# Performance work log

Hardware: AMD Instinct MI355X
Metric: run time of the kernel (lower is better)

## Reference

```python
import jax, jax.numpy as jnp
import numpy as np

EPS = 1e-5
SLOPE = 0.2

def _lrelu(x):
    return jnp.where(x >= 0, x, SLOPE * x)

def _bn(x, axes):
    # BatchNorm in training mode with gamma=1, beta=0 (module defaults), biased var
    m = jnp.mean(x, axis=axes, keepdims=True)
    v = jnp.var(x, axis=axes, keepdims=True)
    return (x - m) * jax.lax.rsqrt(v + EPS)

def _knn(x, k):
    # x: [B, C, N] -> idx [B, N, k] of nearest neighbors (incl. self)
    inner = -2.0 * jnp.einsum('bcn,bcm->bnm', x, x)
    xx = jnp.sum(x * x, axis=1)  # [B, N]
    d = -xx[:, :, None] - inner - xx[:, None, :]  # negative squared dist
    return jax.lax.top_k(d, k)[1]

def _graph_feature(x, k):
    # x: [B, C, N] -> [B, 2C, N, k] of (neighbor - center, center)
    idx = _knn(x, k)                       # [B, N, k]
    xt = jnp.transpose(x, (0, 2, 1))       # [B, N, C]
    feat = jax.vmap(lambda xb, ib: xb[ib])(xt, idx)  # [B, N, k, C]
    center = xt[:, :, None, :]
    out = jnp.concatenate([feat - center, jnp.broadcast_to(center, feat.shape)], axis=-1)
    return jnp.transpose(out, (0, 3, 1, 2))

def _conv2(w, x):   # 1x1 conv2d: x [B,C,N,K]
    return jnp.einsum('oc,bcnk->bonk', w, x)

def _conv1(w, x):   # 1x1 conv1d: x [B,C,N]
    return jnp.einsum('oc,bcn->bon', w, x)

def _pool(xyz, feature, wp, bp, kp):
    # dropout is identity in eval mode
    proj = _conv1(wp, feature) + bp[None, :, None]     # [B, C, N]
    vector = jnp.max(proj, axis=-1, keepdims=True)     # [B, C, 1]
    scores = jax.nn.sigmoid(jnp.sum(feature * vector, axis=1))  # [B, N]
    values, idx = jax.lax.top_k(scores, kp)            # [B, kp]
    node_static = jnp.take_along_axis(xyz, idx[:, None, :], axis=2)
    node_feature = jnp.take_along_axis(feature, idx[:, None, :], axis=2)
    v = values[:, None, :]
    return node_static * v, node_feature * v


def setup_inputs() -> dict:
    key = jax.random.key(0)
    ks = jax.random.split(key, 20)
    def rn(i, shape, s=0.05):
        return jax.random.normal(ks[i], shape, dtype=jnp.float32) * s
    return {
        'x': jax.random.normal(ks[0], (16, 3, 2048), dtype=jnp.float32),
        'w1': rn(1, (64, 6)), 'w2': rn(2, (64, 128)), 'w2m': rn(3, (1024, 128)),
        'w3': rn(4, (128, 256)), 'w4': rn(5, (128, 256)), 'w4m': rn(6, (1024, 256)),
        'w5': rn(7, (256, 512)), 'w5m': rn(8, (1024, 256)),
        'wp1': rn(9, (128, 128)), 'bp1': rn(10, (128,)),
        'wp2': rn(11, (256, 256)), 'bp2': rn(12, (256,)),
        'wl1': rn(13, (512, 3072)),
        'wl2': rn(14, (256, 512)), 'bl2': rn(15, (256,)),
        'wl3': rn(16, (40, 256)), 'bl3': rn(17, (40,)),
    }


def reference(x, w1, w2, w2m, w3, w4, w4m, w5, w5m, wp1, bp1, wp2, bp2, wl1, wl2, bl2, wl3, bl3):
    k = 20
    xyz = x
    # stage 1 (N=2048)
    h = _lrelu(_bn(_conv2(w1, _graph_feature(x, k)), (0, 2, 3)))
    x1 = jnp.max(h, axis=-1)                       # [B, 64, N]
    h = _lrelu(_bn(_conv2(w2, _graph_feature(x1, k)), (0, 2, 3)))
    x2 = jnp.max(h, axis=-1)                       # [B, 64, N]
    xt1_ = jnp.concatenate([x1, x2], axis=1)       # [B, 128, N]
    xt1 = _lrelu(_bn(_conv1(w2m, xt1_), (0, 2)))   # [B, 1024, N]
    node1, nf1 = _pool(xyz, xt1_, wp1, bp1, 256)   # [B,3,256], [B,128,256]
    # stage 2 (256 nodes, k//2)
    h = _lrelu(_bn(_conv2(w3, _graph_feature(nf1, k // 2)), (0, 2, 3)))
    x3 = jnp.max(h, axis=-1)                       # [B, 128, 256]
    h = _lrelu(_bn(_conv2(w4, _graph_feature(x3, k // 2)), (0, 2, 3)))
    x4 = jnp.max(h, axis=-1)
    xt2_ = jnp.concatenate([x3, x4], axis=1)       # [B, 256, 256]
    xt2 = _lrelu(_bn(_conv1(w4m, xt2_), (0, 2)))   # [B, 1024, 256]
    node2, nf2 = _pool(node1, xt2_, wp2, bp2, 64)  # [B,3,64], [B,256,64]
    # stage 3 (64 nodes, k//4)
    h = _lrelu(_bn(_conv2(w5, _graph_feature(nf2, k // 4)), (0, 2, 3)))
    x5 = jnp.max(h, axis=-1)                       # [B, 256, 64]
    xt3 = _lrelu(_bn(_conv1(w5m, x5), (0, 2)))     # [B, 1024, 64]
    # global max pools + head (dropout = identity in eval)
    g = jnp.concatenate([jnp.max(xt1, -1), jnp.max(xt2, -1), jnp.max(xt3, -1)], axis=1)  # [B, 3072]
    h = _lrelu(_bn(g @ wl1.T, (0,)))
    h = _lrelu(_bn(h @ wl2.T + bl2, (0,)))
    out = h @ wl3.T + bl3                          # [B, 40]
    return (out, node1, node2)
```

## Files before the change

kernel.cpp:

```cpp
#include <hip/hip_runtime.h>
#include <cmath>
#include <cstdint>
#include <cstddef>

typedef unsigned int u32;
typedef unsigned short u16;
typedef unsigned long long u64;
typedef __attribute__((ext_vector_type(8))) short short8v;
typedef __attribute__((ext_vector_type(4))) float f32x4;

#define TPB 256
#define EPSV 1e-5f
#define SLP 0.2f

__device__ __forceinline__ float lrelu(float x){ return x >= 0.f ? x : SLP*x; }
__device__ __forceinline__ u32 encf(float f){ u32 u=__float_as_uint(f); return (u&0x80000000u)? ~u : (u|0x80000000u); }
__device__ __forceinline__ float decf(u32 e){ return (e&0x80000000u)? __uint_as_float(e&0x7FFFFFFFu) : __uint_as_float(~e); }
__device__ __forceinline__ u16 f2b(float f){ u32 u=__float_as_uint(f); return (u16)((u + 0x7FFFu + ((u>>16)&1u))>>16); }
__device__ __forceinline__ float b2f(u16 h){ return __uint_as_float(((u32)h)<<16); }

__global__ void k_detect(const u16* __restrict__ raw, int n, int* __restrict__ flag){
  __shared__ float red[TPB];
  int tid=threadIdx.x; float m=0.f;
  for(int i=tid;i<n;i+=TPB){
    float v=fabsf(b2f(raw[i]));
    if(!isnan(v) && !isinf(v) && v>m) m=v;
  }
  red[tid]=m; __syncthreads();
  for(int s=TPB/2;s>0;s>>=1){ if(tid<s) red[tid]=fmaxf(red[tid],red[tid+s]); __syncthreads(); }
  if(tid==0) *flag = (red[0] > 1000.f) ? 1 : 0;
}

struct CvtArgs{ const void* s[18]; float* d[18]; int n[18]; };
__global__ void k_cvt_all(CvtArgs a, const int* __restrict__ flag){
  int z=blockIdx.y; int n=a.n[z]; int f=*flag;
  const void* s=a.s[z]; float* d=a.d[z];
  for(int i=blockIdx.x*TPB+threadIdx.x; i<n; i+=gridDim.x*TPB)
    d[i] = f ? ((const float*)s)[i] : b2f(((const u16*)s)[i]);
}

__global__ void k_castw(const float* __restrict__ W, u16* __restrict__ Wb, int n){
  int i=blockIdx.x*TPB+threadIdx.x; if(i<n) Wb[i]=f2b(W[i]);
}

__global__ void k_xpose_bf(const float* __restrict__ X, u16* __restrict__ Xb,
                           int ldC, int C, int N){
  __shared__ float t[32][33];
  int b=blockIdx.z;
  int c0=blockIdx.y*32, n0=blockIdx.x*32;
  int tx=threadIdx.x&31, ty=threadIdx.x>>5;
  const float* Xs = X + (size_t)b*ldC*N;
  #pragma unroll
  for(int i=0;i<4;i++){
    int c=c0+ty+i*8;
    t[ty+i*8][tx] = (c<C && n0+tx<N) ? Xs[(size_t)c*N + n0+tx] : 0.f;
  }
  __syncthreads();
  u16* Ob = Xb + (size_t)b*N*C;
  #pragma unroll
  for(int i=0;i<4;i++){
    int n=n0+ty+i*8;
    if(n<N && c0+tx<C) Ob[(size_t)n*C + c0+tx] = f2b(t[tx][ty+i*8]);
  }
}

template<int KSTEPS>
__global__ __launch_bounds__(256) void k_convmax_mfma(
    const u16* __restrict__ Wb, const u16* __restrict__ Xb,
    u32* __restrict__ gmaxEnc, int gstride, int g_off, double* __restrict__ stats,
    int C, int N, int O){
  int tid=threadIdx.x, lane=tid&63, w=tid>>6;
  int b=blockIdx.z;
  int oW = blockIdx.y*64 + w*16;
  int nB = blockIdx.x*256;
  int row16 = lane&15, grp = lane>>4;
  short8v af[KSTEPS];
  const u16* Wrow = Wb + (size_t)(oW + row16)*C + grp*8;
  #pragma unroll
  for(int ks=0;ks<KSTEPS;ks++) af[ks] = *(const short8v*)(Wrow + ks*32);
  const short8v zb = {0,0,0,0,0,0,0,0};
  f32x4 acc[16];
  #pragma unroll
  for(int t=0;t<16;t++){
    int n = nB + t*16 + row16;
    bool nv = (n < N);
    const u16* Xrow = Xb + ((size_t)b*N + (nv? n:0))*C + grp*8;
    short8v bf[KSTEPS];
    #pragma unroll
    for(int ks=0;ks<KSTEPS;ks++) bf[ks] = nv ? *(const short8v*)(Xrow + ks*32) : zb;
    f32x4 a = {0.f,0.f,0.f,0.f};
    #pragma unroll
    for(int ks=0;ks<KSTEPS;ks++)
      a = __builtin_amdgcn_mfma_f32_16x16x32_bf16(af[ks], bf[ks], a, 0, 0, 0);
    acc[t]=a;
  }
  float mxr[4], s1r[4], s2r[4];
  #pragma unroll
  for(int r=0;r<4;r++){ mxr[r]=-INFINITY; s1r[r]=0.f; s2r[r]=0.f; }
  #pragma unroll
  for(int t=0;t<16;t++){
    int n = nB + t*16 + row16;
    bool nv = (n<N);
    #pragma unroll
    for(int r=0;r<4;r++){
      float y = acc[t][r];
      if(nv){ mxr[r]=fmaxf(mxr[r],y); s1r[r]+=y; s2r[r]+=y*y; }
    }
  }
  #pragma unroll
  for(int s=1;s<16;s<<=1){
    #pragma unroll
    for(int r=0;r<4;r++){
      mxr[r]=fmaxf(mxr[r], __shfl_xor(mxr[r], s));
      s1r[r]+=__shfl_xor(s1r[r], s);
      s2r[r]+=__shfl_xor(s2r[r], s);
    }
  }
  if(row16==0){
    #pragma unroll
    for(int r=0;r<4;r++){
      int o = oW + grp*4 + r;
      atomicMax(&gmaxEnc[(size_t)b*gstride + g_off + o], encf(mxr[r]));
      atomicAdd(&stats[2*o], (double)s1r[r]);
      atomicAdd(&stats[2*o+1], (double)s2r[r]);
    }
  }
}

__global__ void k_sqnorm(const float* __restrict__ X, float* __restrict__ xx, int B, int ldC, int C, int N){
  int i=blockIdx.x*TPB+threadIdx.x; if(i>=B*N) return;
  int b=i/N, n=i-b*N;
  const float* p = X + ((size_t)b*ldC)*N + n;
  float s=0.f;
  for(int c=0;c<C;c++){ float x=p[(size_t)c*N]; s+=x*x; }
  xx[i]=s;
}

template<int JMAX, int CT>
__global__ __launch_bounds__(256) void k_knn_fused(
    const float* __restrict__ X, const float* __restrict__ xx,
    int ldC, int KSEL, int* __restrict__ idxOut){
  const int N = JMAX*64;
  extern __shared__ float sm[];
  __shared__ u64 cand[4][128];
  int tid=threadIdx.x, lane=tid&63, w=tid>>6;
  int b=blockIdx.y, row0=blockIdx.x*4;
  const float* Xb = X + (size_t)b*ldC*N;
  const float* xxb = xx + (size_t)b*N;

  if constexpr (JMAX==32){
    int c0 = tid*4;
    float4 acc0[4], acc1[4];
    #pragma unroll
    for(int r=0;r<4;r++){ acc0[r]=make_float4(0,0,0,0); acc1[r]=make_float4(0,0,0,0); }
    #pragma unroll 4
    for(int c=0;c<CT;c++){
      const float* Xc = Xb + (size_t)c*N;
      float4 b0 = *(const float4*)&Xc[c0];
      float4 b1 = *(const float4*)&Xc[c0+1024];
      #pragma unroll
      for(int r=0;r<4;r++){
        float a = Xc[row0+r];
        acc0[r].x += a*b0.x; acc0[r].y += a*b0.y; acc0[r].z += a*b0.z; acc0[r].w += a*b0.w;
        acc1[r].x += a*b1.x; acc1[r].y += a*b1.y; acc1[r].z += a*b1.z; acc1[r].w += a*b1.w;
      }
    }
    float4 xm0 = *(const float4*)&xxb[c0];
    float4 xm1 = *(const float4*)&xxb[c0+1024];
    #pragma unroll
    for(int r=0;r<4;r++){
      float xr = xxb[row0+r];
      float4 d0, d1;
      d0.x=2.f*acc0[r].x-xr-xm0.x; d0.y=2.f*acc0[r].y-xr-xm0.y;
      d0.z=2.f*acc0[r].z-xr-xm0.z; d0.w=2.f*acc0[r].w-xr-xm0.w;
      d1.x=2.f*acc1[r].x-xr-xm1.x; d1.y=2.f*acc1[r].y-xr-xm1.y;
      d1.z=2.f*acc1[r].z-xr-xm1.z; d1.w=2.f*acc1[r].w-xr-xm1.w;
      *(float4*)&sm[r*N + c0]        = d0;
      *(float4*)&sm[r*N + c0 + 1024] = d1;
    }
  } else {
    int tcol = (tid < N)? tid : (tid & (N-1));
    float acc[4];
    #pragma unroll
    for(int r=0;r<4;r++) acc[r]=0.f;
    #pragma unroll 4
    for(int c=0;c<CT;c++){
      const float* Xc = Xb + (size_t)c*N;
      float bv = Xc[tcol];
      #pragma unroll
      for(int r=0;r<4;r++) acc[r] += Xc[row0+r]*bv;
    }
    float xm = xxb[tcol];
    #pragma unroll
    for(int r=0;r<4;r++) sm[r*N + tcol] = 2.f*acc[r] - xxb[row0+r] - xm;
  }
  __syncthreads();

  u64* cw = cand[w];
  int r = w;
  const float* Sr = sm + (size_t)r*N;
  u32 ev[JMAX];
  if constexpr (JMAX>=4){
    #pragma unroll
    for(int ch=0;ch<JMAX/4;ch++){
      float4 v = *(const float4*)&Sr[ch*256 + lane*4];
      ev[ch*4+0]=encf(v.x); ev[ch*4+1]=encf(v.y); ev[ch*4+2]=encf(v.z); ev[ch*4+3]=encf(v.w);
    }
  } else {
    ev[0]=encf(Sr[lane]);
  }
  int* op = idxOut + ((size_t)b*N + row0 + r)*KSEL;
  if constexpr (JMAX>=8){
    u32 vmax=ev[0];
    #pragma unroll
    for(int j=1;j<JMAX;j++) vmax = vmax>ev[j]? vmax:ev[j];
    u32 lo=0u, hi=0xFFFFFFFFu;
    while(lo<hi){
      u32 d=hi-lo; u32 mid=lo+(d>>1)+(d&1u);
      int cnum=(int)__popcll(__ballot(vmax>=mid));
      if(cnum>=KSEL) lo=mid; else hi=mid-1u;
    }
    u32 T=lo;
    u64 lml=((u64)1<<lane)-1ull;
    u32 base=0;
    #pragma unroll
    for(int j=0;j<JMAX;j++){
      bool p = ev[j]>=T;
      u64 mk=__ballot(p);
      u32 pos=base+(u32)__popcll(mk&lml);
      int m = (j>>2)*256 + lane*4 + (j&3);
      if(p && pos<128u) cw[pos] = ((u64)ev[j]<<32) | (u64)(u32)(~(u32)m);
      base += (u32)__popcll(mk);
    }
    int nc=(int)base;
    if(nc<=64){
      u64 cv = cw[lane];
      if(lane>=nc) cv=0ull;
      #pragma unroll
      for(int kk=2;kk<=64;kk<<=1){
        #pragma unroll
        for(int jj=kk>>1;jj>0;jj>>=1){
          u64 p=__shfl_xor(cv,jj);
          bool takeMax=(((lane&jj)!=0)==((lane&kk)==0));
          u64 mx=cv>p?cv:p, mn=cv>p?p:cv;
          cv=takeMax?mx:mn;
        }
      }
      if(lane>=64-KSEL) op[63-lane]=(int)(~(u32)cv);
    } else if(nc<=128){
      u64 c0v=cw[lane], c1v=cw[64+lane];
      if(64+lane>=nc) c1v=0ull;
      u64 kl=~0ull;
      for(int t=0;t<KSEL;t++){
        u64 bk=(c0v<kl)?c0v:0ull;
        if(c1v<kl&&c1v>bk) bk=c1v;
        #pragma unroll
        for(int s=1;s<64;s<<=1){u64 ok=__shfl_xor(bk,s); if(ok>bk)bk=ok;}
        if(lane==0) op[t]=(int)(~(u32)bk);
        kl=bk;
      }
    } else {
      u64 kl=~0ull;
      for(int t=0;t<KSEL;t++){
        u64 bk=0ull;
        #pragma unroll
        for(int j=0;j<JMAX;j++){
          int m = (j>>2)*256 + lane*4 + (j&3);
          u64 kj=((u64)ev[j]<<32)|(u64)(u32)(~(u32)m);
          if(kj<kl&&kj>bk) bk=kj;
        }
        #pragma unroll
        for(int s=1;s<64;s<<=1){u64 ok=__shfl_xor(bk,s); if(ok>bk)bk=ok;}
        if(lane==0) op[t]=(int)(~(u32)bk);
        kl=bk;
      }
    }
  } else {
    u64 key[JMAX];
    #pragma unroll
    for(int j=0;j<JMAX;j++){
      int m = (JMAX>=4)? ((j>>2)*256 + lane*4 + (j&3)) : lane;
      key[j]=((u64)ev[j]<<32)|(u64)(u32)(~(u32)m);
    }
    u64 kl=~0ull;
    for(int t=0;t<KSEL;t++){
      u64 bk=0ull;
      #pragma unroll
      for(int j=0;j<JMAX;j++){ u64 kj=key[j]; if(kj<kl&&kj>bk) bk=kj; }
      #pragma unroll
      for(int s=1;s<64;s<<=1){u64 ok=__shfl_xor(bk,s); if(ok>bk)bk=ok;}
      if(lane==0) op[t]=(int)(~(u32)bk);
      kl=bk;
    }
  }
}

__global__ void k_topk_sort(const float* __restrict__ S, int M, int K,
                            int* __restrict__ idxOut, float* __restrict__ valOut){
  extern __shared__ u64 key[];
  int b=blockIdx.x, tid=threadIdx.x;
  const float* Sr = S + (size_t)b*M;
  for(int i=tid;i<M;i+=TPB)
    key[i] = ((u64)(~encf(Sr[i]))<<32) | (u32)i;
  __syncthreads();
  for(int k=2;k<=M;k<<=1){
    for(int j=k>>1;j>0;j>>=1){
      for(int i=tid;i<M;i+=TPB){
        int ixj=i^j;
        if(ixj>i){
          u64 a=key[i], c=key[ixj];
          bool up=((i&k)==0);
          if(up ? (a>c) : (a<c)){ key[i]=c; key[ixj]=a; }
        }
      }
      __syncthreads();
    }
  }
  for(int p=tid;p<K;p+=TPB){
    u64 kk=key[p];
    idxOut[(size_t)b*K+p]=(int)(u32)(kk&0xFFFFFFFFull);
    valOut[(size_t)b*K+p]=decf(~(u32)(kk>>32));
  }
}

__global__ void k_uv(const float* __restrict__ X, int ldC, const float* __restrict__ W,
                     float* __restrict__ U, float* __restrict__ V, int C, int N, int O){
  int n=blockIdx.x*TPB+threadIdx.x; if(n>=N) return;
  int o=blockIdx.y, b=blockIdx.z;
  const float* Xb = X + ((size_t)b*ldC)*N + n;
  const float* Wr = W + (size_t)o*2*C;
  float u=0,v=0;
  for(int c=0;c<C;c++){ float x=Xb[(size_t)c*N]; float wa=Wr[c], wb=Wr[C+c]; u+=wa*x; v+=(wb-wa)*x; }
  size_t off=((size_t)b*O+o)*N+n; U[off]=u; V[off]=v;
}

template<int KT, int OT>
__global__ void k_nbr_t(const float* __restrict__ U, const float* __restrict__ V, const int* __restrict__ idx,
                        float* __restrict__ outBase, int ldCout, int ch_off,
                        double* __restrict__ stats, int O, int N){
  __shared__ double redS[4][OT], redQ[4][OT];
  int tid=threadIdx.x, lane=tid&63, wv=tid>>6;
  int n = blockIdx.x*TPB+tid;
  int o0 = blockIdx.y*OT, b = blockIdx.z;
  bool act = (n<N);
  int nc = act? n : (N-1);
  int jr[KT];
  const int* jp = idx + ((size_t)b*N+nc)*KT;
  #pragma unroll
  for(int k=0;k<KT;k++){ int j=jp[k]; jr[k] = ((unsigned)j<(unsigned)N)? j : 0; }
  for(int oo=0;oo<OT;oo++){
    const float* Ur = U + ((size_t)b*O+o0+oo)*N;
    float mx=-INFINITY, s1=0.f, s2=0.f;
    #pragma unroll
    for(int k=0;k<KT;k++){ float u=Ur[jr[k]]; mx=fmaxf(mx,u); s1+=u; s2+=u*u; }
    float v = V[((size_t)b*O+o0+oo)*N+nc];
    if(act) outBase[((size_t)b*ldCout+ch_off+o0+oo)*N+n] = mx+v;
    double cs = act ? ((double)s1 + (double)KT*(double)v) : 0.0;
    double cq = act ? ((double)s2 + 2.0*(double)v*(double)s1 + (double)KT*(double)v*(double)v) : 0.0;
    #pragma unroll
    for(int s=1;s<64;s<<=1){ cs += __shfl_xor(cs,s); cq += __shfl_xor(cq,s); }
    if(lane==0){ redS[wv][oo]=cs; redQ[wv][oo]=cq; }
  }
  __syncthreads();
  if(tid<OT){
    double s=0,q=0;
    #pragma unroll
    for(int w=0;w<4;w++){ s+=redS[w][tid]; q+=redQ[w][tid]; }
    atomicAdd(&stats[2*(o0+tid)], s);
    atomicAdd(&stats[2*(o0+tid)+1], q);
  }
}

__global__ void k_bnact(float* __restrict__ out, int ldCout, int ch_off, const double* __restrict__ stats,
                        int O, int N, double cnt){
  int n=blockIdx.x*TPB+threadIdx.x; if(n>=N) return;
  int o=blockIdx.y, b=blockIdx.z;
  double m=stats[2*o]/cnt;
  double var=stats[2*o+1]/cnt - m*m;
  float s=rsqrtf((float)var+EPSV);
  size_t p=((size_t)b*ldCout+ch_off+o)*N+n;
  float h=out[p];
  out[p] = lrelu((float)((double)h-m)*s);
}

template<int PTS>
__global__ void k_convmax(const float* __restrict__ X, int ldC, const float* __restrict__ W, const float* __restrict__ bias,
                          u32* __restrict__ gmaxEnc, int gstride, int g_off, double* __restrict__ stats,
                          int C, int N, int O){
  __shared__ float red[4*16*3];
  int tid=threadIdx.x, ot=blockIdx.y, b=blockIdx.z;
  int lane=tid&63, wv=tid>>6;
  int n0 = blockIdx.x*TPB*PTS + tid*PTS;
  bool act = (n0 < N);
  int n0c = act ? n0 : (N-PTS);
  const float* Xb = X + ((size_t)b*ldC)*N;
  const float* Wr = W + (size_t)ot*16*C;
  float acc[16][PTS];
  #pragma unroll
  for(int oo=0;oo<16;oo++)
    #pragma unroll
    for(int p=0;p<PTS;p++) acc[oo][p]=0.f;
  for(int c=0;c<C;c+=4){
    float xv[4][PTS];
    #pragma unroll
    for(int cc=0;cc<4;cc++){
      if(PTS==4){
        float4 t = *(const float4*)&Xb[(size_t)(c+cc)*N + n0c];
        xv[cc][0]=t.x; xv[cc][1]=t.y; xv[cc][2]=t.z; xv[cc][3]=t.w;
      } else {
        xv[cc][0]=Xb[(size_t)(c+cc)*N + n0c];
      }
    }
    #pragma unroll
    for(int oo=0;oo<16;oo++){
      float w0=Wr[oo*C+c], w1=Wr[oo*C+c+1], w2=Wr[oo*C+c+2], w3=Wr[oo*C+c+3];
      #pragma unroll
      for(int p=0;p<PTS;p++)
        acc[oo][p] += w0*xv[0][p] + w1*xv[1][p] + w2*xv[2][p] + w3*xv[3][p];
    }
  }
  bool hs = (stats!=nullptr);
  #pragma unroll
  for(int oo=0;oo<16;oo++){
    float bval = bias? bias[ot*16+oo] : 0.f;
    float mx=-INFINITY, s1=0.f, s2=0.f;
    #pragma unroll
    for(int p=0;p<PTS;p++){
      float y=acc[oo][p]+bval;
      if(act && n0+p<N){ mx=fmaxf(mx,y); s1+=y; s2+=y*y; }
    }
    #pragma unroll
    for(int s=1;s<64;s<<=1){
      mx=fmaxf(mx,__shfl_xor(mx,s));
      if(hs){ s1+=__shfl_xor(s1,s); s2+=__shfl_xor(s2,s); }
    }
    if(lane==0){ red[(wv*16+oo)*3]=mx; red[(wv*16+oo)*3+1]=s1; red[(wv*16+oo)*3+2]=s2; }
  }
  __syncthreads();
  if(tid<16){
    int oo=tid, o=ot*16+oo;
    float mx=red[oo*3], s1=red[oo*3+1], s2=red[oo*3+2];
    #pragma unroll
    for(int w=1;w<4;w++){ mx=fmaxf(mx,red[(w*16+oo)*3]); s1+=red[(w*16+oo)*3+1]; s2+=red[(w*16+oo)*3+2]; }
    atomicMax(&gmaxEnc[(size_t)b*gstride+g_off+o], encf(mx));
    if(hs){ atomicAdd(&stats[2*o],(double)s1); atomicAdd(&stats[2*o+1],(double)s2); }
  }
}

__global__ void k_gfinal(const u32* __restrict__ gmaxEnc, int gstride, int g_off, const double* __restrict__ stats,
                         float* __restrict__ G, int B, int O, double cnt){
  int i=blockIdx.x*TPB+threadIdx.x; if(i>=B*O) return;
  int b=i/O, o=i-b*O;
  double m=stats[2*o]/cnt;
  double var=stats[2*o+1]/cnt - m*m;
  float s=rsqrtf((float)var+EPSV);
  float x=decf(gmaxEnc[(size_t)b*gstride+g_off+o]);
  G[(size_t)b*gstride+g_off+o]=lrelu((float)((double)x-m)*s);
}

__global__ void k_scores(const float* __restrict__ X, int ldC, const u32* __restrict__ vecEnc,
                         float* __restrict__ sc, int C, int N){
  int n=blockIdx.x*TPB+threadIdx.x; if(n>=N) return;
  int b=blockIdx.y;
  const float* Xb = X + ((size_t)b*ldC)*N + n;
  double s=0;
  for(int c=0;c<C;c++) s += (double)Xb[(size_t)c*N]*(double)decf(vecEnc[(size_t)b*C+c]);
  float sf=(float)s;
  sc[(size_t)b*N+n]=1.f/(1.f+expf(-sf));
}

__global__ void k_pgather(const float* __restrict__ xyz, int ldCx, const float* __restrict__ feat, int ldCf,
                          const int* __restrict__ pidx, const float* __restrict__ pval,
                          float* __restrict__ nodeOut, float* __restrict__ nfOut, int Cf, int Nin, int Kp){
  int b=blockIdx.y;
  int i=blockIdx.x*TPB+threadIdx.x;
  int total=(3+Cf)*Kp; if(i>=total) return;
  int c=i/Kp, p=i-c*Kp;
  int j=pidx[(size_t)b*Kp+p]; if((unsigned)j>=(unsigned)Nin) j=0;
  float v=pval[(size_t)b*Kp+p];
  if(c<3) nodeOut[((size_t)b*3+c)*Kp+p]=xyz[((size_t)b*ldCx+c)*Nin+j]*v;
  else { int cf=c-3; nfOut[((size_t)b*Cf+cf)*Kp+p]=feat[((size_t)b*ldCf+cf)*Nin+j]*v; }
}

__global__ void k_fc_wave(const float* __restrict__ A, const float* __restrict__ W, const float* __restrict__ bias,
                          float* __restrict__ Y, int B, int IN, int OUT){
  int gw = (blockIdx.x*blockDim.x + threadIdx.x) >> 6;
  if(gw >= B*OUT) return;
  int lane = threadIdx.x & 63;
  int b = gw/OUT, j = gw - b*OUT;
  const float4* a4 = (const float4*)(A + (size_t)b*IN);
  const float4* w4 = (const float4*)(W + (size_t)j*IN);
  int n4 = IN >> 2;
  float s = 0.f;
  for(int t=lane; t<n4; t+=64){
    float4 av=a4[t], wv=w4[t];
    s += av.x*wv.x + av.y*wv.y + av.z*wv.z + av.w*wv.w;
  }
  #pragma unroll
  for(int sh=1; sh<64; sh<<=1) s += __shfl_xor(s, sh);
  if(lane==0) Y[gw] = s + (bias? bias[j]:0.f);
}

__global__ void k_bnb(const float* __restrict__ Y, float* __restrict__ H, int B, int F){
  int f=blockIdx.x*TPB+threadIdx.x; if(f>=F) return;
  double s=0,q=0;
  for(int b=0;b<B;b++){ double y=Y[(size_t)b*F+f]; s+=y; q+=y*y; }
  double m=s/B, var=q/B-m*m;
  float sc=rsqrtf((float)var+EPSV);
  for(int b=0;b<B;b++){ float y=Y[(size_t)b*F+f]; H[(size_t)b*F+f]=lrelu((float)((double)y-m)*sc); }
}

__global__ void k_out(const float* __restrict__ OUTF, const float* __restrict__ N1v, const float* __restrict__ N2v,
                      void* __restrict__ dout, const int* __restrict__ flag){
  int i=blockIdx.x*TPB+threadIdx.x; if(i>=16000) return;
  float v = (i<640)? OUTF[i] : (i<12928)? N1v[i-640] : N2v[i-12928];
  if(*flag) ((float*)dout)[i]=v; else ((u16*)dout)[i]=f2b(v);
}

extern "C" void kernel_launch(void* const* d_in, const int* in_sizes, int n_in,
                              void* d_out, int out_size, void* d_ws, size_t ws_size,
                              hipStream_t stream){
  const int B=16;
  char* basep=(char*)d_ws; size_t off=0;
  auto alloc=[&](size_t elems, size_t esz)->void*{
    off=(off+255)&~(size_t)255; void* p=basep+off; off+=elems*esz; return p;
  };
  const int NINP=18;
  const int insz[NINP]={98304,384,8192,131072,32768,32768,262144,131072,262144,16384,128,65536,256,1572864,131072,256,10240,40};
  float* F[NINP];
  for(int i=0;i<NINP;i++) F[i]=(float*)alloc((size_t)insz[i],4);
  float* XF=F[0];
  float *W1F=F[1],*W2F=F[2],*W2MF=F[3],*W3F=F[4],*W4F=F[5],*W4MF=F[6],*W5F=F[7],*W5MF=F[8],
        *WP1F=F[9],*BP1F=F[10],*WP2F=F[11],*BP2F=F[12],*WL1F=F[13],*WL2F=F[14],*BL2F=F[15],*WL3F=F[16],*BL3F=F[17];
  float* XX  =(float*)alloc((size_t)16*2048,4);
  float* U   =(float*)alloc((size_t)16*64*2048,4);
  float* V   =(float*)alloc((size_t)16*64*2048,4);
  float* XT1 =(float*)alloc((size_t)16*128*2048,4);
  float* XT2 =(float*)alloc((size_t)16*256*256,4);
  float* NF1 =(float*)alloc((size_t)16*128*256,4);
  float* NF2 =(float*)alloc((size_t)16*256*64,4);
  float* X5  =(float*)alloc((size_t)16*256*64,4);
  float* NODE1=(float*)alloc((size_t)16*3*256,4);
  float* NODE2=(float*)alloc((size_t)16*3*64,4);
  float* SCORES=(float*)alloc((size_t)16*2048,4);
  float* PVAL1=(float*)alloc((size_t)16*256,4);
  float* PVAL2=(float*)alloc((size_t)16*64,4);
  float* G   =(float*)alloc((size_t)16*3072,4);
  float* Y1  =(float*)alloc((size_t)16*512,4);
  float* H1  =(float*)alloc((size_t)16*512,4);
  float* Y2  =(float*)alloc((size_t)16*256,4);
  float* H2  =(float*)alloc((size_t)16*256,4);
  float* OUTF=(float*)alloc((size_t)16*40,4);
  u32* GMAX  =(u32*)alloc((size_t)16*3072,4);
  u32* VECENC=(u32*)alloc((size_t)16*256,4);
  int* IDX   =(int*)alloc((size_t)16*2048*20,4);
  int* PIDX1 =(int*)alloc((size_t)16*256,4);
  int* PIDX2 =(int*)alloc((size_t)16*64,4);
  double* STATS=(double*)alloc((size_t)2*1024,8);
  int* FLAG  =(int*)alloc(64,4);
  u16* XTB  =(u16*)alloc((size_t)16*2048*128,2);
  u16* WB2M =(u16*)alloc((size_t)131072,2);
  u16* WB4M =(u16*)alloc((size_t)262144,2);
  u16* WB5M =(u16*)alloc((size_t)262144,2);

  k_detect<<<dim3(1),dim3(TPB),0,stream>>>((const u16*)d_in[1], insz[1], FLAG);
  CvtArgs ca;
  for(int i=0;i<NINP;i++){ ca.s[i]=d_in[i]; ca.d[i]=F[i]; ca.n[i]=insz[i]; }
  k_cvt_all<<<dim3(64,NINP),dim3(TPB),0,stream>>>(ca, FLAG);
  k_castw<<<dim3((131072+TPB-1)/TPB),dim3(TPB),0,stream>>>(W2MF,WB2M,131072);
  k_castw<<<dim3((262144+TPB-1)/TPB),dim3(TPB),0,stream>>>(W4MF,WB4M,262144);
  k_castw<<<dim3((262144+TPB-1)/TPB),dim3(TPB),0,stream>>>(W5MF,WB5M,262144);

  auto knn=[&](const float* X, int ldC, int C, int N, int K){
    k_sqnorm<<<dim3((B*N+TPB-1)/TPB),dim3(TPB),0,stream>>>(X,XX,B,ldC,C,N);
    size_t shm=(size_t)4*N*4;
    if(N==2048 && C==3)       k_knn_fused<32,3>  <<<dim3(N/4,B),dim3(256),shm,stream>>>(X,XX,ldC,K,IDX);
    else if(N==2048)          k_knn_fused<32,64> <<<dim3(N/4,B),dim3(256),shm,stream>>>(X,XX,ldC,K,IDX);
    else if(N==256)           k_knn_fused<4,128> <<<dim3(N/4,B),dim3(256),shm,stream>>>(X,XX,ldC,K,IDX);
    else                      k_knn_fused<1,256> <<<dim3(N/4,B),dim3(256),shm,stream>>>(X,XX,ldC,K,IDX);
  };

  auto graph_conv=[&](const float* X, int ldC, int C, int N, int K, const float* W, int O,
                      float* outBase, int ldCout, int ch_off){
    knn(X,ldC,C,N,K);
    k_uv<<<dim3((N+TPB-1)/TPB,O,B),dim3(TPB),0,stream>>>(X,ldC,W,U,V,C,N,O);
    hipMemsetAsync(STATS,0,2*(size_t)O*sizeof(double),stream);
    dim3 g((N+TPB-1)/TPB, O/8, B);
    if(K==20)      k_nbr_t<20,8><<<g,dim3(TPB),0,stream>>>(U,V,IDX,outBase,ldCout,ch_off,STATS,O,N);
    else if(K==10) k_nbr_t<10,8><<<g,dim3(TPB),0,stream>>>(U,V,IDX,outBase,ldCout,ch_off,STATS,O,N);
    else           k_nbr_t<5,8> <<<g,dim3(TPB),0,stream>>>(U,V,IDX,outBase,ldCout,ch_off,STATS,O,N);
    double cnt=(double)B*(double)N*(double)K;
    k_bnact<<<dim3((N+TPB-1)/TPB,O,B),dim3(TPB),0,stream>>>(outBase,ldCout,ch_off,STATS,O,N,cnt);
  };

  auto convmax_f32=[&](const float* X,int ldC,const float* W,const float* bias,
                   u32* gmax,int gstride,int g_off,double* stats,int C,int N,int O){
    if(N>=1024) k_convmax<4><<<dim3((N+TPB*4-1)/(TPB*4),O/16,B),dim3(TPB),0,stream>>>(X,ldC,W,bias,gmax,gstride,g_off,stats,C,N,O);
    else        k_convmax<1><<<dim3((N+TPB-1)/TPB,O/16,B),dim3(TPB),0,stream>>>(X,ldC,W,bias,gmax,gstride,g_off,stats,C,N,O);
  };

  auto pool=[&](const float* xyzF,int ldCx,const float* featF,int ldCf,int Cf,int Nin,
                const float* WP,const float* BP,int Op,int Kp,
                float* nodeOut,float* nfOut,int* pidx,float* pval){
    hipMemsetAsync(VECENC,0,(size_t)B*Op*4,stream);
    convmax_f32(featF,ldCf,WP,BP,VECENC,Op,0,(double*)nullptr,Cf,Nin,Op);
    k_scores<<<dim3((Nin+TPB-1)/TPB,B),dim3(TPB),0,stream>>>(featF,ldCf,VECENC,SCORES,Cf,Nin);
    k_topk_sort<<<dim3(B),dim3(TPB),(size_t)Nin*8,stream>>>(SCORES,Nin,Kp,pidx,pval);
    k_pgather<<<dim3(((3+Cf)*Kp+TPB-1)/TPB,B),dim3(TPB),0,stream>>>(xyzF,ldCx,featF,ldCf,pidx,pval,nodeOut,nfOut,Cf,Nin,Kp);
  };

  auto gseg=[&](const float* X,int ldC,int C,int N,const u16* WBc,int g_off,double cnt){
    hipMemsetAsync(STATS,0,2*1024*sizeof(double),stream);
    k_xpose_bf<<<dim3((N+31)/32,(C+31)/32,B),dim3(256),0,stream>>>(X,XTB,ldC,C,N);
    dim3 g((N+255)/256, 1024/64, B);
    if(C==128) k_convmax_mfma<4><<<g,dim3(256),0,stream>>>(WBc,XTB,GMAX,3072,g_off,STATS,C,N,1024);
    else       k_convmax_mfma<8><<<g,dim3(256),0,stream>>>(WBc,XTB,GMAX,3072,g_off,STATS,C,N,1024);
    k_gfinal<<<dim3((B*1024+TPB-1)/TPB),dim3(TPB),0,stream>>>(GMAX,3072,g_off,STATS,G,B,1024,cnt);
  };

  graph_conv(XF,3,3,2048,20,W1F,64,XT1,128,0);
  graph_conv(XT1,128,64,2048,20,W2F,64,XT1,128,64);
  hipMemsetAsync(GMAX,0,(size_t)16*3072*4,stream);
  gseg(XT1,128,128,2048,WB2M,0,(double)16*2048);
  pool(XF,3,XT1,128,128,2048,WP1F,BP1F,128,256,NODE1,NF1,PIDX1,PVAL1);
  graph_conv(NF1,128,128,256,10,W3F,128,XT2,256,0);
  graph_conv(XT2,256,128,256,10,W4F,128,XT2,256,128);
  gseg(XT2,256,256,256,WB4M,1024,(double)16*256);
  pool(NODE1,3,XT2,256,256,256,WP2F,BP2F,256,64,NODE2,NF2,PIDX2,PVAL2);
  graph_conv(NF2,256,256,64,5,W5F,256,X5,256,0);
  gseg(X5,256,256,64,WB5M,2048,(double)16*64);
  k_fc_wave<<<dim3((16*512*64+TPB-1)/TPB),dim3(TPB),0,stream>>>(G,WL1F,(const float*)nullptr,Y1,16,3072,512);
  k_bnb<<<dim3((512+TPB-1)/TPB),dim3(TPB),0,stream>>>(Y1,H1,16,512);
  k_fc_wave<<<dim3((16*256*64+TPB-1)/TPB),dim3(TPB),0,stream>>>(H1,WL2F,BL2F,Y2,16,512,256);
  k_bnb<<<dim3((256+TPB-1)/TPB),dim3(TPB),0,stream>>>(Y2,H2,16,256);
  k_fc_wave<<<dim3((16*40*64+TPB-1)/TPB),dim3(TPB),0,stream>>>(H2,WL3F,BL3F,OUTF,16,256,40);
  k_out<<<dim3((16000+TPB-1)/TPB),dim3(TPB),0,stream>>>(OUTF,NODE1,NODE2,(u16*)d_out,FLAG);
}
```

Measured before the change: 1.172 ms.

## Add register-resident KNN kernel for N=2048 with one wavefront per row

Adds a new KNN kernel for the 2048-point stages where each wavefront owns one query row and keeps all 2048 distances in registers (32 per lane), broadcasting the row's coordinates via shuffles. The old version staged a 4-row distance tile in 32 KB of shared memory, and the new kernel drops that staging and selects top-k with a ballot-based threshold binary search plus in-register compaction and a wave sort. The cost is higher register pressure under a launch_bounds occupancy hint, and each wavefront now re-reads the whole column feature set without the 4-row reuse the old tile had. The old JMAX==32 branch in the fused kernel is removed because it is no longer used.

```diff
diff --git a/kernel.cpp b/kernel.cpp
--- a/kernel.cpp
+++ b/kernel.cpp
@@ -136,6 +136,122 @@
   xx[i]=s;
 }
 
+template<int CT>
+__global__ __launch_bounds__(256, 5) void k_knn_reg(
+    const float* __restrict__ X, const float* __restrict__ xx,
+    int ldC, int KSEL, int* __restrict__ idxOut){
+  const int N = 2048;
+  __shared__ u64 cand[4][128];
+  int tid=threadIdx.x, lane=tid&63, w=tid>>6;
+  int b=blockIdx.y, row=blockIdx.x*4+w;
+  const float* Xb  = X  + (size_t)b*ldC*N;
+  const float* xxb = xx + (size_t)b*N;
+
+  float av = (lane < CT) ? Xb[(size_t)lane*N + row] : 0.f;
+
+  float4 acc[8];
+  #pragma unroll
+  for(int ch=0;ch<8;ch++) acc[ch]=make_float4(0.f,0.f,0.f,0.f);
+  const float* Xl = Xb + lane*4;
+
+#define KNN_ACC_STEP(c) { \
+    float a = __shfl(av, (c)); \
+    const float* Xc = Xl + (size_t)(c)*N; \
+    _Pragma("unroll") \
+    for(int ch=0;ch<8;ch++){ \
+      float4 bv = *(const float4*)(Xc + ch*256); \
+      acc[ch].x += a*bv.x; acc[ch].y += a*bv.y; \
+      acc[ch].z += a*bv.z; acc[ch].w += a*bv.w; \
+    } }
+
+  if constexpr (CT <= 4){
+    #pragma unroll
+    for(int c=0;c<CT;c++) KNN_ACC_STEP(c)
+  } else {
+    #pragma unroll 2
+    for(int c=0;c<CT;c++) KNN_ACC_STEP(c)
+  }
+#undef KNN_ACC_STEP
+
+  float xr = xxb[row];
+  u32 ev[32];
+  #pragma unroll
+  for(int ch=0;ch<8;ch++){
+    float4 xm = *(const float4*)&xxb[ch*256 + lane*4];
+    ev[ch*4+0]=encf(2.f*acc[ch].x - xr - xm.x);
+    ev[ch*4+1]=encf(2.f*acc[ch].y - xr - xm.y);
+    ev[ch*4+2]=encf(2.f*acc[ch].z - xr - xm.z);
+    ev[ch*4+3]=encf(2.f*acc[ch].w - xr - xm.w);
+  }
+
+  u64* cw = cand[w];
+  int* op = idxOut + ((size_t)b*N + row)*KSEL;
+  u32 vmax=ev[0];
+  #pragma unroll
+  for(int j=1;j<32;j++) vmax = vmax>ev[j]? vmax:ev[j];
+  u32 lo=0u, hi=0xFFFFFFFFu;
+  while(lo<hi){
+    u32 d=hi-lo; u32 mid=lo+(d>>1)+(d&1u);
+    int cnum=(int)__popcll(__ballot(vmax>=mid));
+    if(cnum>=KSEL) lo=mid; else hi=mid-1u;
+  }
+  u32 T=lo;
+  u64 lml=((u64)1<<lane)-1ull;
+  u32 base=0;
+  #pragma unroll
+  for(int j=0;j<32;j++){
+    bool p = ev[j]>=T;
+    u64 mk=__ballot(p);
+    u32 pos=base+(u32)__popcll(mk&lml);
+    int m = (j>>2)*256 + lane*4 + (j&3);
+    if(p && pos<128u) cw[pos] = ((u64)ev[j]<<32) | (u64)(u32)(~(u32)m);
+    base += (u32)__popcll(mk);
+  }
+  int nc=(int)base;
+  if(nc<=64){
+    u64 cv = cw[lane];
+    if(lane>=nc) cv=0ull;
+    #pragma unroll
+    for(int kk=2;kk<=64;kk<<=1){
+      #pragma unroll
+      for(int jj=kk>>1;jj>0;jj>>=1){
+        u64 p=__shfl_xor(cv,jj);
+        bool takeMax=(((lane&jj)!=0)==((lane&kk)==0));
+        u64 mx=cv>p?cv:p, mn=cv>p?p:cv;
+        cv=takeMax?mx:mn;
+      }
+    }
+    if(lane>=64-KSEL) op[63-lane]=(int)(~(u32)cv);
+  } else if(nc<=128){
+    u64 c0v=cw[lane], c1v=cw[64+lane];
+    if(64+lane>=nc) c1v=0ull;
+    u64 kl=~0ull;
+    for(int t=0;t<KSEL;t++){
+      u64 bk=(c0v<kl)?c0v:0ull;
+      if(c1v<kl&&c1v>bk) bk=c1v;
+      #pragma unroll
+      for(int s=1;s<64;s<<=1){u64 ok=__shfl_xor(bk,s); if(ok>bk)bk=ok;}
+      if(lane==0) op[t]=(int)(~(u32)bk);
+      kl=bk;
+    }
+  } else {
+    u64 kl=~0ull;
+    for(int t=0;t<KSEL;t++){
+      u64 bk=0ull;
+      #pragma unroll
+      for(int j=0;j<32;j++){
+        int m = (j>>2)*256 + lane*4 + (j&3);
+        u64 kj=((u64)ev[j]<<32)|(u64)(u32)(~(u32)m);
+        if(kj<kl&&kj>bk) bk=kj;
+      }
+      #pragma unroll
+      for(int s=1;s<64;s<<=1){u64 ok=__shfl_xor(bk,s); if(ok>bk)bk=ok;}
+      if(lane==0) op[t]=(int)(~(u32)bk);
+      kl=bk;
+    }
+  }
+}
+
 template<int JMAX, int CT>
 __global__ __launch_bounds__(256) void k_knn_fused(
     const float* __restrict__ X, const float* __restrict__ xx,
@@ -148,37 +264,7 @@
   const float* Xb = X + (size_t)b*ldC*N;
   const float* xxb = xx + (size_t)b*N;
 
-  if constexpr (JMAX==32){
-    int c0 = tid*4;
-    float4 acc0[4], acc1[4];
-    #pragma unroll
-    for(int r=0;r<4;r++){ acc0[r]=make_float4(0,0,0,0); acc1[r]=make_float4(0,0,0,0); }
-    #pragma unroll 4
-    for(int c=0;c<CT;c++){
-      const float* Xc = Xb + (size_t)c*N;
-      float4 b0 = *(const float4*)&Xc[c0];
-      float4 b1 = *(const float4*)&Xc[c0+1024];
-      #pragma unroll
-      for(int r=0;r<4;r++){
-        float a = Xc[row0+r];
-        acc0[r].x += a*b0.x; acc0[r].y += a*b0.y; acc0[r].z += a*b0.z; acc0[r].w += a*b0.w;
-        acc1[r].x += a*b1.x; acc1[r].y += a*b1.y; acc1[r].z += a*b1.z; acc1[r].w += a*b1.w;
-      }
-    }
-    float4 xm0 = *(const float4*)&xxb[c0];
-    float4 xm1 = *(const float4*)&xxb[c0+1024];
-    #pragma unroll
-    for(int r=0;r<4;r++){
-      float xr = xxb[row0+r];
-      float4 d0, d1;
-      d0.x=2.f*acc0[r].x-xr-xm0.x; d0.y=2.f*acc0[r].y-xr-xm0.y;
-      d0.z=2.f*acc0[r].z-xr-xm0.z; d0.w=2.f*acc0[r].w-xr-xm0.w;
-      d1.x=2.f*acc1[r].x-xr-xm1.x; d1.y=2.f*acc1[r].y-xr-xm1.y;
-      d1.z=2.f*acc1[r].z-xr-xm1.z; d1.w=2.f*acc1[r].w-xr-xm1.w;
-      *(float4*)&sm[r*N + c0]        = d0;
-      *(float4*)&sm[r*N + c0 + 1024] = d1;
-    }
-  } else {
+  {
     int tcol = (tid < N)? tid : (tid & (N-1));
     float acc[4];
     #pragma unroll
@@ -573,11 +659,15 @@
 
   auto knn=[&](const float* X, int ldC, int C, int N, int K){
     k_sqnorm<<<dim3((B*N+TPB-1)/TPB),dim3(TPB),0,stream>>>(X,XX,B,ldC,C,N);
-    size_t shm=(size_t)4*N*4;
-    if(N==2048 && C==3)       k_knn_fused<32,3>  <<<dim3(N/4,B),dim3(256),shm,stream>>>(X,XX,ldC,K,IDX);
-    else if(N==2048)          k_knn_fused<32,64> <<<dim3(N/4,B),dim3(256),shm,stream>>>(X,XX,ldC,K,IDX);
-    else if(N==256)           k_knn_fused<4,128> <<<dim3(N/4,B),dim3(256),shm,stream>>>(X,XX,ldC,K,IDX);
-    else                      k_knn_fused<1,256> <<<dim3(N/4,B),dim3(256),shm,stream>>>(X,XX,ldC,K,IDX);
+    if(N==2048 && C==3)       k_knn_reg<3>  <<<dim3(N/4,B),dim3(256),0,stream>>>(X,XX,ldC,K,IDX);
+    else if(N==2048)          k_knn_reg<64> <<<dim3(N/4,B),dim3(256),0,stream>>>(X,XX,ldC,K,IDX);
+    else if(N==256){
+      size_t shm=(size_t)4*N*4;
+      k_knn_fused<4,128> <<<dim3(N/4,B),dim3(256),shm,stream>>>(X,XX,ldC,K,IDX);
+    } else {
+      size_t shm=(size_t)4*N*4;
+      k_knn_fused<1,256> <<<dim3(N/4,B),dim3(256),shm,stream>>>(X,XX,ldC,K,IDX);
+    }
   };
 
   auto graph_conv=[&](const float* X, int ldC, int C, int N, int K, const float* W, int O,
```

Measured after the change: 1.501 ms. 28.1% more time.
